# Kernel tuning notes

Measured on AMD Instinct MI355X. Metric: run time of the kernel, lower is better.

The kernel has to match this reference:

```python
import jax, jax.numpy as jnp
import numpy as np

PADDED_NODE_ID = -1
B, N, F = 4096, 128, 64


def setup_inputs() -> dict:
    key = jax.random.key(0)
    k1, k2, k3, k4, k5, k6 = jax.random.split(key, 6)
    src_ids = jax.random.randint(k1, (B, N), 0, 1000, dtype=jnp.int64 if jax.config.jax_enable_x64 else jnp.int32)
    dst_ids = jax.random.randint(k2, (B, N), 0, 1000, dtype=src_ids.dtype)
    w1 = jax.random.normal(k3, (F, 1), dtype=jnp.float32) * 0.1
    b1 = jax.random.normal(k4, (F,), dtype=jnp.float32) * 0.1
    w2 = jax.random.normal(k5, (F, F), dtype=jnp.float32) * 0.1
    b2 = jax.random.normal(k6, (F,), dtype=jnp.float32) * 0.1
    return {"src_neighbour_nodes_ids": src_ids, "dst_neighbour_nodes_ids": dst_ids,
            "w1": w1, "b1": b1, "w2": w2, "b2": b2}


def _pairwise_count(a, b):
    # count[b, i] = #{ j : a[b, i] == b[b, j] }  -- batched histogram via equality
    eq = a[:, :, None] == b[:, None, :]  # [B, N, N] bool
    return eq.sum(axis=-1).astype(jnp.float32)


def _mlp(freq, w1, b1, w2, b2):
    # freq: [B, N, 2] -> Linear(1,F) -> ReLU -> Linear(F,F), then sum over dim 2
    h = freq[..., None] * w1[:, 0] + b1          # [B, N, 2, F]
    h = jax.nn.relu(h)
    out = jnp.einsum('bncf,gf->bncg', h, w2) + b2  # [B, N, 2, F]
    return out.sum(axis=2)                        # [B, N, F]


def reference(src_neighbour_nodes_ids, dst_neighbour_nodes_ids, w1, b1, w2, b2):
    src, dst = src_neighbour_nodes_ids, dst_neighbour_nodes_ids
    src_in_src = _pairwise_count(src, src)
    dst_in_dst = _pairwise_count(dst, dst)
    src_in_dst = _pairwise_count(src, dst)
    dst_in_src = _pairwise_count(dst, src)

    src_pad = (src == PADDED_NODE_ID)[..., None]
    dst_pad = (dst == PADDED_NODE_ID)[..., None]
    source_freq = jnp.where(src_pad, 0.0, jnp.stack([src_in_src, src_in_dst], axis=-1))  # [B,N,2]
    dst_freq = jnp.where(dst_pad, 0.0, jnp.stack([dst_in_dst, dst_in_src], axis=-1))      # [B,N,2]

    src_feat = _mlp(source_freq, w1, b1, w2, b2)
    dst_feat = _mlp(dst_freq, w1, b1, w2, b2)
    return src_feat, dst_feat
```

## Files before the change

kernel.cpp:

```cpp
#include <hip/hip_runtime.h>

#define BATCH 4096
#define NN 128
#define FF 64
#define NC 129
#define PADDED_ID (-1)

__global__ void build_table_kernel(const float* __restrict__ w1,
                                   const float* __restrict__ b1,
                                   const float* __restrict__ w2,
                                   const float* __restrict__ b2,
                                   float* __restrict__ table) {
    int c = blockIdx.x;
    int g = threadIdx.x;
    float cf = (float)c;
    float acc = b2[g];
    #pragma unroll
    for (int f = 0; f < FF; ++f) {
        float h = cf * w1[f] + b1[f];
        h = h > 0.0f ? h : 0.0f;
        acc += h * w2[g * FF + f];
    }
    table[c * FF + g] = acc;
}

__global__ __launch_bounds__(256)
void encode_kernel(const int* __restrict__ src,
                   const int* __restrict__ dst,
                   const float* __restrict__ table,
                   float* __restrict__ out) {
    __shared__ int s_src[NN];
    __shared__ int s_dst[NN];
    __shared__ int s_cA[256];
    __shared__ int s_cB[256];
    __shared__ float s_tab[NC * FF];

    const int b   = blockIdx.x;
    const int tid = threadIdx.x;

    if (tid < NN) s_src[tid] = src[b * NN + tid];
    else          s_dst[tid - NN] = dst[b * NN + (tid - NN)];

    {
        const float4* tg = (const float4*)table;
        float4* ts = (float4*)s_tab;
        #pragma unroll
        for (int idx = tid; idx < (NC * FF) / 4; idx += 256)
            ts[idx] = tg[idx];
    }
    __syncthreads();

    {
        const int i = tid & (NN - 1);
        const int* A  = (tid < NN) ? s_src : s_dst;
        const int* Bp = (tid < NN) ? s_dst : s_src;
        const int my = A[i];
        int ca = 0, cb = 0;
        #pragma unroll 8
        for (int j = 0; j < NN; ++j) {
            ca += (my == A[j]);
            cb += (my == Bp[j]);
        }
        if (my == PADDED_ID) { ca = 0; cb = 0; }
        s_cA[tid] = ca;
        s_cB[tid] = cb;
    }
    __syncthreads();

    const int g4 = tid & 15;
    const int n0 = tid >> 4;
    const float4* tab4 = (const float4*)s_tab;
    float4* out_src = (float4*)out + (size_t)b * NN * (FF / 4);
    float4* out_dst = (float4*)out + (size_t)BATCH * NN * (FF / 4) + (size_t)b * NN * (FF / 4);

    #pragma unroll
    for (int n = n0; n < NN; n += 16) {
        {
            const int c0 = s_cA[n], c1 = s_cB[n];
            float4 v0 = tab4[c0 * (FF / 4) + g4];
            float4 v1 = tab4[c1 * (FF / 4) + g4];
            float4 r;
            r.x = v0.x + v1.x; r.y = v0.y + v1.y;
            r.z = v0.z + v1.z; r.w = v0.w + v1.w;
            out_src[n * (FF / 4) + g4] = r;
        }
        {
            const int c0 = s_cA[n + NN], c1 = s_cB[n + NN];
            float4 v0 = tab4[c0 * (FF / 4) + g4];
            float4 v1 = tab4[c1 * (FF / 4) + g4];
            float4 r;
            r.x = v0.x + v1.x; r.y = v0.y + v1.y;
            r.z = v0.z + v1.z; r.w = v0.w + v1.w;
            out_dst[n * (FF / 4) + g4] = r;
        }
    }
}

extern "C" void kernel_launch(void* const* d_in, const int* in_sizes, int n_in,
                              void* d_out, int out_size, void* d_ws, size_t ws_size,
                              hipStream_t stream) {
    const int*   src = (const int*)d_in[0];
    const int*   dst = (const int*)d_in[1];
    const float* w1  = (const float*)d_in[2];
    const float* b1  = (const float*)d_in[3];
    const float* w2  = (const float*)d_in[4];
    const float* b2  = (const float*)d_in[5];
    float* out   = (float*)d_out;
    float* table = (float*)d_ws;

    build_table_kernel<<<NC, FF, 0, stream>>>(w1, b1, w2, b2, table);
    encode_kernel<<<BATCH, 256, 0, stream>>>(src, dst, table, out);
}
```

Before: 281.2 us.

## Process four batches per block to amortize table staging; vectorize count loop

Each block now handles four batch rows, so the 33KB lookup table is copied into LDS once per four rows instead of once per row, cutting redundant global/L2 reads and LDS fills. The pairwise count loop reads ids as int4 broadcasts from LDS. The trade-off is a grid of 1024 blocks instead of 4096 and extra barriers per row, which may reduce latency hiding and overlap of stores across blocks.

```diff
diff --git a/kernel.cpp b/kernel.cpp
--- a/kernel.cpp
+++ b/kernel.cpp
@@ -5,6 +5,8 @@
 #define FF 64
 #define NC 129
 #define PADDED_ID (-1)
+#define BPB 4
+#define GRID (BATCH / BPB)
 
 __global__ void build_table_kernel(const float* __restrict__ w1,
                                    const float* __restrict__ b1,
@@ -29,17 +31,12 @@
                    const int* __restrict__ dst,
                    const float* __restrict__ table,
                    float* __restrict__ out) {
-    __shared__ int s_src[NN];
-    __shared__ int s_dst[NN];
-    __shared__ int s_cA[256];
-    __shared__ int s_cB[256];
     __shared__ float s_tab[NC * FF];
+    __shared__ int   s_ids[2 * NN];
+    __shared__ int   s_cA[2 * NN];
+    __shared__ int   s_cB[2 * NN];
 
-    const int b   = blockIdx.x;
     const int tid = threadIdx.x;
-
-    if (tid < NN) s_src[tid] = src[b * NN + tid];
-    else          s_dst[tid - NN] = dst[b * NN + (tid - NN)];
 
     {
         const float4* tg = (const float4*)table;
@@ -48,50 +45,63 @@
         for (int idx = tid; idx < (NC * FF) / 4; idx += 256)
             ts[idx] = tg[idx];
     }
-    __syncthreads();
-
-    {
-        const int i = tid & (NN - 1);
-        const int* A  = (tid < NN) ? s_src : s_dst;
-        const int* Bp = (tid < NN) ? s_dst : s_src;
-        const int my = A[i];
-        int ca = 0, cb = 0;
-        #pragma unroll 8
-        for (int j = 0; j < NN; ++j) {
-            ca += (my == A[j]);
-            cb += (my == Bp[j]);
-        }
-        if (my == PADDED_ID) { ca = 0; cb = 0; }
-        s_cA[tid] = ca;
-        s_cB[tid] = cb;
-    }
-    __syncthreads();
 
     const int g4 = tid & 15;
     const int n0 = tid >> 4;
     const float4* tab4 = (const float4*)s_tab;
-    float4* out_src = (float4*)out + (size_t)b * NN * (FF / 4);
-    float4* out_dst = (float4*)out + (size_t)BATCH * NN * (FF / 4) + (size_t)b * NN * (FF / 4);
 
-    #pragma unroll
-    for (int n = n0; n < NN; n += 16) {
+    for (int k = 0; k < BPB; ++k) {
+        const int b = blockIdx.x * BPB + k;
+
+        __syncthreads();
+        if (tid < NN) s_ids[tid]      = src[b * NN + tid];
+        else          s_ids[tid]      = dst[b * NN + (tid - NN)];
+        __syncthreads();
+
         {
-            const int c0 = s_cA[n], c1 = s_cB[n];
-            float4 v0 = tab4[c0 * (FF / 4) + g4];
-            float4 v1 = tab4[c1 * (FF / 4) + g4];
-            float4 r;
-            r.x = v0.x + v1.x; r.y = v0.y + v1.y;
-            r.z = v0.z + v1.z; r.w = v0.w + v1.w;
-            out_src[n * (FF / 4) + g4] = r;
+            const int i  = tid & (NN - 1);
+            const int*  A  = (tid < NN) ? s_ids : s_ids + NN;
+            const int*  Bp = (tid < NN) ? s_ids + NN : s_ids;
+            const int my = A[i];
+            const int4* A4 = (const int4*)A;
+            const int4* B4 = (const int4*)Bp;
+            int ca = 0, cb = 0;
+            #pragma unroll
+            for (int j = 0; j < NN / 4; ++j) {
+                int4 a = A4[j];
+                int4 bb = B4[j];
+                ca += (my == a.x) + (my == a.y) + (my == a.z) + (my == a.w);
+                cb += (my == bb.x) + (my == bb.y) + (my == bb.z) + (my == bb.w);
+            }
+            if (my == PADDED_ID) { ca = 0; cb = 0; }
+            s_cA[tid] = ca;
+            s_cB[tid] = cb;
         }
-        {
-            const int c0 = s_cA[n + NN], c1 = s_cB[n + NN];
-            float4 v0 = tab4[c0 * (FF / 4) + g4];
-            float4 v1 = tab4[c1 * (FF / 4) + g4];
-            float4 r;
-            r.x = v0.x + v1.x; r.y = v0.y + v1.y;
-            r.z = v0.z + v1.z; r.w = v0.w + v1.w;
-            out_dst[n * (FF / 4) + g4] = r;
+        __syncthreads();
+
+        float4* out_src = (float4*)out + (size_t)b * (NN * FF / 4);
+        float4* out_dst = (float4*)out + (size_t)BATCH * (NN * FF / 4)
+                                       + (size_t)b * (NN * FF / 4);
+        #pragma unroll
+        for (int n = n0; n < NN; n += 16) {
+            {
+                const int c0 = s_cA[n], c1 = s_cB[n];
+                float4 v0 = tab4[c0 * (FF / 4) + g4];
+                float4 v1 = tab4[c1 * (FF / 4) + g4];
+                float4 r;
+                r.x = v0.x + v1.x; r.y = v0.y + v1.y;
+                r.z = v0.z + v1.z; r.w = v0.w + v1.w;
+                out_src[n * (FF / 4) + g4] = r;
+            }
+            {
+                const int c0 = s_cA[NN + n], c1 = s_cB[NN + n];
+                float4 v0 = tab4[c0 * (FF / 4) + g4];
+                float4 v1 = tab4[c1 * (FF / 4) + g4];
+                float4 r;
+                r.x = v0.x + v1.x; r.y = v0.y + v1.y;
+                r.z = v0.z + v1.z; r.w = v0.w + v1.w;
+                out_dst[n * (FF / 4) + g4] = r;
+            }
         }
     }
 }
@@ -109,5 +119,5 @@
     float* table = (float*)d_ws;
 
     build_table_kernel<<<NC, FF, 0, stream>>>(w1, b1, w2, b2, table);
-    encode_kernel<<<BATCH, 256, 0, stream>>>(src, dst, table, out);
+    encode_kernel<<<GRID, 256, 0, stream>>>(src, dst, table, out);
 }
```

Measured after the change: 277.8 us. No clear change (-1.2%).
